# Kernel tuning notes

Measured on AMD Instinct MI355X. Metric: run time of the kernel, lower is better.

The kernel has to match this reference:

```python
import jax, jax.numpy as jnp
import numpy as np

EPS = 1e-6
ROPE_THETA = 1000000.0
SPAN_LENGTHS = [700, 300, 600, 448]
L, D, H, HK, DH, FF = 2, 2048, 16, 8, 128, 8192


def _rmsnorm(x, w):
    var = jnp.mean(jnp.square(x), axis=-1, keepdims=True)
    return x * jax.lax.rsqrt(var + EPS) * w


def _rotate_half(x):
    x1, x2 = jnp.split(x, 2, axis=-1)
    return jnp.concatenate([-x2, x1], axis=-1)


def setup_inputs() -> dict:
    key = jax.random.key(0)
    ks = jax.random.split(key, 8)
    s = 0.02  # init scale
    seg = np.repeat(np.arange(len(SPAN_LENGTHS), dtype=np.int32), SPAN_LENGTHS)
    pos = np.concatenate([np.arange(n, dtype=np.int32) for n in SPAN_LENGTHS])
    T = seg.shape[0]
    return {
        "hidden_states": jax.random.normal(ks[0], (T, D), jnp.float32),
        "ln1_w": jnp.ones((L, D), jnp.float32),
        "ln2_w": jnp.ones((L, D), jnp.float32),
        "wq": jax.random.normal(ks[1], (L, D, H * DH), jnp.float32) * s,
        "wk": jax.random.normal(ks[2], (L, D, HK * DH), jnp.float32) * s,
        "wv": jax.random.normal(ks[3], (L, D, HK * DH), jnp.float32) * s,
        "wo": jax.random.normal(ks[4], (L, H * DH, D), jnp.float32) * s,
        "qn_w": jnp.ones((L, DH), jnp.float32),
        "kn_w": jnp.ones((L, DH), jnp.float32),
        "wg": jax.random.normal(ks[5], (L, D, FF), jnp.float32) * s,
        "wu": jax.random.normal(ks[6], (L, D, FF), jnp.float32) * s,
        "wd": jax.random.normal(ks[7], (L, FF, D), jnp.float32) * s,
        "final_norm_w": jnp.ones((D,), jnp.float32),
        "segment_ids": jnp.asarray(seg),
        "position_ids": jnp.asarray(pos),
    }


def reference(hidden_states, ln1_w, ln2_w, wq, wk, wv, wo, qn_w, kn_w, wg, wu, wd, final_norm_w, segment_ids, position_ids):
    T = hidden_states.shape[0]
    # rotary tables from per-request positions (positions reset per span)
    inv_freq = 1.0 / (ROPE_THETA ** (jnp.arange(0, DH, 2, dtype=jnp.float32) / DH))
    freqs = position_ids.astype(jnp.float32)[:, None] * inv_freq  # [T, DH/2]
    emb = jnp.concatenate([freqs, freqs], axis=-1)                # [T, DH]
    cos = jnp.cos(emb)[:, None, :]
    sin = jnp.sin(emb)[:, None, :]
    # ragged causal mask: attend only within the same request span, causally
    tok = jnp.arange(T)
    mask = (segment_ids[:, None] == segment_ids[None, :]) & (tok[:, None] >= tok[None, :])
    neg = jnp.finfo(hidden_states.dtype).min
    scale = 1.0 / np.sqrt(DH)

    x = hidden_states
    for l in range(L):
        h = _rmsnorm(x, ln1_w[l])
        q = (h @ wq[l]).reshape(T, H, DH)
        k = (h @ wk[l]).reshape(T, HK, DH)
        v = (h @ wv[l]).reshape(T, HK, DH)
        q = _rmsnorm(q, qn_w[l])  # Qwen3 per-head q/k RMSNorm
        k = _rmsnorm(k, kn_w[l])
        q = q * cos + _rotate_half(q) * sin
        k = k * cos + _rotate_half(k) * sin
        rep = H // HK  # GQA
        k = jnp.repeat(k, rep, axis=1)
        v = jnp.repeat(v, rep, axis=1)
        scores = jnp.einsum('thd,shd->hts', q, k) * scale  # [H, T, T]
        scores = jnp.where(mask[None], scores, neg)
        attn = jax.nn.softmax(scores, axis=-1)
        o = jnp.einsum('hts,shd->thd', attn, v).reshape(T, H * DH)
        x = x + o @ wo[l]
        h = _rmsnorm(x, ln2_w[l])
        x = x + (jax.nn.silu(h @ wg[l]) * (h @ wu[l])) @ wd[l]
    return _rmsnorm(x, final_norm_w)
```

## Files before the change

### kernel.cpp

```cpp
#include <hip/hip_runtime.h>
#include <stdint.h>

#define T_SEQ 2048
#define DMODEL 2048
#define NH 16
#define NKV 8
#define DHEAD 128
#define DFF 8192

typedef float f32x4 __attribute__((ext_vector_type(4)));
typedef float f32x2 __attribute__((ext_vector_type(2)));
typedef __bf16 bf16x8 __attribute__((ext_vector_type(8)));
typedef unsigned short ushort_t;

typedef __attribute__((address_space(1))) void gvoid;
typedef __attribute__((address_space(3))) void lvoid;

__device__ inline unsigned short f2bf(float f) {
  unsigned int u = __float_as_uint(f);
  u += 0x7fffu + ((u >> 16) & 1u);
  return (unsigned short)(u >> 16);
}
__device__ inline float bf2f(unsigned short h) {
  return __uint_as_float(((unsigned int)h) << 16);
}

__device__ inline void gload_lds16(const void* g, void* l) {
  __builtin_amdgcn_global_load_lds((gvoid*)g, (lvoid*)l, 16, 0, 0);
}

template <typename TIN>
__global__ __launch_bounds__(256) void k_transpose_bf16(const TIN* __restrict__ in,
                                                        ushort_t* __restrict__ out,
                                                        int R, int C) {
  __shared__ float tile[64 * 72];
  int tid = threadIdx.x;
  int r0 = blockIdx.y * 64, c0 = blockIdx.x * 64;
  int rl = tid >> 4;
  int cc = tid & 15;
#pragma unroll
  for (int i = 0; i < 4; ++i) {
    int row = rl + i * 16;
    const TIN* src = in + (size_t)(r0 + row) * C + c0 + cc * 4;
    float v0, v1, v2, v3;
    if constexpr (sizeof(TIN) == 4) {
      f32x4 v = *(const f32x4*)src;
      v0 = v.x; v1 = v.y; v2 = v.z; v3 = v.w;
    } else {
      ushort4 v = *(const ushort4*)src;
      v0 = bf2f(v.x); v1 = bf2f(v.y); v2 = bf2f(v.z); v3 = bf2f(v.w);
    }
    int chunk = cc ^ (row & 15);
    f32x4 t = {v0, v1, v2, v3};
    *(f32x4*)&tile[row * 72 + chunk * 4] = t;
  }
  __syncthreads();
#pragma unroll
  for (int i = 0; i < 4; ++i) {
    int nrow = rl + i * 16;
    int k4 = cc * 4;
    ushort4 o;
    {
      int k = k4 + 0;
      o.x = f2bf(tile[k * 72 + (((nrow >> 2) ^ (k & 15)) << 2) + (nrow & 3)]);
      k = k4 + 1;
      o.y = f2bf(tile[k * 72 + (((nrow >> 2) ^ (k & 15)) << 2) + (nrow & 3)]);
      k = k4 + 2;
      o.z = f2bf(tile[k * 72 + (((nrow >> 2) ^ (k & 15)) << 2) + (nrow & 3)]);
      k = k4 + 3;
      o.w = f2bf(tile[k * 72 + (((nrow >> 2) ^ (k & 15)) << 2) + (nrow & 3)]);
    }
    *(ushort4*)(out + (size_t)(c0 + nrow) * R + r0 + k4) = o;
  }
}

template <int BF16OUT>
__global__ __launch_bounds__(256) void k_rmsnorm(const float* __restrict__ X,
                                                 const float* __restrict__ W,
                                                 void* __restrict__ OUT) {
  int row = blockIdx.x, tid = threadIdx.x;
  const float* xr = X + (size_t)row * DMODEL;
  f32x4 x0 = *(const f32x4*)(xr + tid * 4);
  f32x4 x1 = *(const f32x4*)(xr + 1024 + tid * 4);
  float ss = x0.x * x0.x + x0.y * x0.y + x0.z * x0.z + x0.w * x0.w +
             x1.x * x1.x + x1.y * x1.y + x1.z * x1.z + x1.w * x1.w;
#pragma unroll
  for (int o = 1; o < 64; o <<= 1) ss += __shfl_xor(ss, o, 64);
  __shared__ float red[4];
  int w = tid >> 6;
  if ((tid & 63) == 0) red[w] = ss;
  __syncthreads();
  float tot = red[0] + red[1] + red[2] + red[3];
  float sc = rsqrtf(tot / (float)DMODEL + 1e-6f);
  f32x4 w0 = *(const f32x4*)(W + tid * 4);
  f32x4 w1 = *(const f32x4*)(W + 1024 + tid * 4);
  if constexpr (BF16OUT) {
    ushort_t* o = (ushort_t*)OUT + (size_t)row * DMODEL;
    ushort4 a, b;
    a.x = f2bf(x0.x * sc * w0.x); a.y = f2bf(x0.y * sc * w0.y);
    a.z = f2bf(x0.z * sc * w0.z); a.w = f2bf(x0.w * sc * w0.w);
    b.x = f2bf(x1.x * sc * w1.x); b.y = f2bf(x1.y * sc * w1.y);
    b.z = f2bf(x1.z * sc * w1.z); b.w = f2bf(x1.w * sc * w1.w);
    *(ushort4*)(o + tid * 4) = a;
    *(ushort4*)(o + 1024 + tid * 4) = b;
  } else {
    float* o = (float*)OUT + (size_t)row * DMODEL;
    f32x4 a = {x0.x * sc * w0.x, x0.y * sc * w0.y, x0.z * sc * w0.z, x0.w * sc * w0.w};
    f32x4 b = {x1.x * sc * w1.x, x1.y * sc * w1.y, x1.z * sc * w1.z, x1.w * sc * w1.w};
    *(f32x4*)(o + tid * 4) = a;
    *(f32x4*)(o + 1024 + tid * 4) = b;
  }
}

__global__ __launch_bounds__(256) void k_red4res(const float* __restrict__ P,
                                                 const float* __restrict__ RES,
                                                 float* __restrict__ OUT, int n) {
  int i = (blockIdx.x * 256 + threadIdx.x) * 4;
  if (i >= n) return;
  f32x4 v = *(const f32x4*)(RES + i);
#pragma unroll
  for (int z = 0; z < 4; ++z) {
    f32x4 t = *(const f32x4*)(P + (size_t)z * n + i);
    v.x += t.x; v.y += t.y; v.z += t.z; v.w += t.w;
  }
  *(f32x4*)(OUT + i) = v;
}

#define EPI_STORE 0
#define EPI_SILU 2
#define EPI_STOREB 3

#define LOAD_B256(bs, rbase)                                                   \
  {                                                                            \
    _Pragma("unroll") for (int ks = 0; ks < 2; ++ks)                           \
        _Pragma("unroll") for (int ni = 0; ni < 2; ++ni)                       \
            bfr[ks][ni] = *(const bf16x8*)((bs) +                              \
                (((rbase) + ni * 16 + lr) << 6) +                              \
                ((((ks << 2) + lg) ^ (lr & 7)) << 3));                         \
  }

#define MFMA_Q256(q)                                                           \
  {                                                                            \
    _Pragma("unroll") for (int ks = 0; ks < 2; ++ks)                           \
        _Pragma("unroll") for (int mi = 0; mi < 4; ++mi)                       \
            _Pragma("unroll") for (int ni = 0; ni < 2; ++ni)                   \
                acc[mi][(q) * 2 + ni] =                                        \
                    __builtin_amdgcn_mfma_f32_16x16x32_bf16(                   \
                        af[ks][mi], bfr[ks][ni], acc[mi][(q) * 2 + ni], 0, 0, 0); \
  }

template <int LAST>
__device__ __forceinline__ void g256_iter(
    const ushort_t* __restrict__ as, const ushort_t* __restrict__ bsA,
    const ushort_t* __restrict__ bsB, ushort_t* __restrict__ nA,
    ushort_t* __restrict__ nB, const ushort_t* __restrict__ an,
    const ushort_t* __restrict__ bn, size_t rs, int slds, int lr, int lg,
    f32x4 (&acc)[4][8]) {
  bf16x8 af[2][4], bfr[2][2];
#pragma unroll
  for (int ks = 0; ks < 2; ++ks)
#pragma unroll
    for (int mi = 0; mi < 4; ++mi)
      af[ks][mi] = *(const bf16x8*)(as + ((mi * 16 + lr) << 6) +
                                    ((((ks << 2) + lg) ^ (lr & 7)) << 3));
  LOAD_B256(bsA, 0);
  if constexpr (!LAST) {
    gload_lds16(an, nA + slds);
    gload_lds16(an + rs, nA + 4096 + slds);
  }
  __builtin_amdgcn_s_barrier();
  asm volatile("s_waitcnt lgkmcnt(0)" ::: "memory");
  __builtin_amdgcn_sched_barrier(0);
  __builtin_amdgcn_s_setprio(1);
  MFMA_Q256(0);
  __builtin_amdgcn_s_setprio(0);
  __builtin_amdgcn_s_barrier();
  LOAD_B256(bsA, 32);
  if constexpr (!LAST) {
    gload_lds16(an + 2 * rs, nA + 8192 + slds);
    gload_lds16(an + 3 * rs, nA + 12288 + slds);
    asm volatile("s_waitcnt vmcnt(4)" ::: "memory");
  } else {
    asm volatile("s_waitcnt vmcnt(0)" ::: "memory");
  }
  __builtin_amdgcn_s_barrier();
  asm volatile("s_waitcnt lgkmcnt(0)" ::: "memory");
  __builtin_amdgcn_sched_barrier(0);
  __builtin_amdgcn_s_setprio(1);
  MFMA_Q256(1);
  __builtin_amdgcn_s_setprio(0);
  __builtin_amdgcn_s_barrier();
  LOAD_B256(bsB, 0);
  if constexpr (!LAST) {
    gload_lds16(bn, nB + slds);
    gload_lds16(bn + 2 * rs, nB + 8192 + slds);
  }
  __builtin_amdgcn_s_barrier();
  asm volatile("s_waitcnt lgkmcnt(0)" ::: "memory");
  __builtin_amdgcn_sched_barrier(0);
  __builtin_amdgcn_s_setprio(1);
  MFMA_Q256(2);
  __builtin_amdgcn_s_setprio(0);
  __builtin_amdgcn_s_barrier();
  LOAD_B256(bsB, 32);
  if constexpr (!LAST) {
    gload_lds16(bn + rs, nB + 4096 + slds);
    gload_lds16(bn + 3 * rs, nB + 12288 + slds);
    asm volatile("s_waitcnt vmcnt(2)" ::: "memory");
  }
  __builtin_amdgcn_s_barrier();
  asm volatile("s_waitcnt lgkmcnt(0)" ::: "memory");
  __builtin_amdgcn_sched_barrier(0);
  __builtin_amdgcn_s_setprio(1);
  MFMA_Q256(3);
  __builtin_amdgcn_s_setprio(0);
  __builtin_amdgcn_s_barrier();
}

template <int EPI>
__global__ __launch_bounds__(512, 2) void k_gemm256(
    const ushort_t* __restrict__ A, const ushort_t* __restrict__ BT,
    const ushort_t* __restrict__ GINB, float* __restrict__ CF,
    ushort_t* __restrict__ CB, int N, int Kstride, int Kc, size_t zoff) {
  __shared__ ushort_t lds[65536];
  const int tid = threadIdx.x;
  const int l = tid & 63, wid = tid >> 6;
  const int wm = wid >> 1, wn = wid & 1;
  const int lr = l & 15, lg = l >> 4;
  const int m0 = blockIdx.y * 256, n0 = blockIdx.x * 256;
  const int z = blockIdx.z;
  const int NT = Kc >> 6;

  A += (size_t)z * Kc;
  BT += (size_t)z * Kc;
  CF += (size_t)z * zoff;

  const int srow = tid >> 3;
  const int scs = (tid & 7) ^ (srow & 7);
  const size_t sgoff = (size_t)srow * Kstride + scs * 8;
  const int slds = wid * 512;

  const ushort_t* ga = A + (size_t)m0 * Kstride + sgoff;
  const ushort_t* gb = BT + (size_t)n0 * Kstride + sgoff;
  const size_t rs = (size_t)64 * Kstride;

  f32x4 acc[4][8] = {};

  ushort_t* Ab0 = lds;
  ushort_t* Bb0 = lds + 16384;
  ushort_t* Ab1 = lds + 32768;
  ushort_t* Bb1 = lds + 49152;

  gload_lds16(ga, Ab0 + slds);
  gload_lds16(ga + rs, Ab0 + 4096 + slds);
  gload_lds16(ga + 2 * rs, Ab0 + 8192 + slds);
  gload_lds16(ga + 3 * rs, Ab0 + 12288 + slds);
  gload_lds16(gb, Bb0 + slds);
  gload_lds16(gb + 2 * rs, Bb0 + 8192 + slds);
  gload_lds16(gb + rs, Bb0 + 4096 + slds);
  gload_lds16(gb + 3 * rs, Bb0 + 12288 + slds);
  asm volatile("s_waitcnt vmcnt(2)" ::: "memory");
  __builtin_amdgcn_s_barrier();

  for (int kt = 0; kt < NT - 1; ++kt) {
    const int d = kt & 1;
    const ushort_t* as = (d ? Ab1 : Ab0) + wm * 4096;
    const ushort_t* bsA = (d ? Bb1 : Bb0) + (wn * 2) * 4096;
    ushort_t* nA = d ? Ab0 : Ab1;
    ushort_t* nB = d ? Bb0 : Bb1;
    g256_iter<0>(as, bsA, bsA + 4096, nA, nB, ga + (size_t)(kt + 1) * 64,
                 gb + (size_t)(kt + 1) * 64, rs, slds, lr, lg, acc);
  }
  {
    const int d = (NT - 1) & 1;
    const ushort_t* as = (d ? Ab1 : Ab0) + wm * 4096;
    const ushort_t* bsA = (d ? Bb1 : Bb0) + (wn * 2) * 4096;
    g256_iter<1>(as, bsA, bsA + 4096, nullptr, nullptr, nullptr, nullptr, rs,
                 slds, lr, lg, acc);
  }

#pragma unroll
  for (int mi = 0; mi < 4; ++mi)
#pragma unroll
    for (int ci = 0; ci < 8; ++ci)
#pragma unroll
      for (int rr = 0; rr < 4; ++rr) {
        int m = m0 + wm * 64 + mi * 16 + lg * 4 + rr;
        int n = n0 + wn * 128 + ci * 16 + lr;
        size_t off = (size_t)m * N + n;
        float v = acc[mi][ci][rr];
        if constexpr (EPI == EPI_STORE) {
          CF[off] = v;
        } else if constexpr (EPI == EPI_STOREB) {
          CB[off] = f2bf(v);
        } else {
          float gv = bf2f(GINB[off]);
          float s = gv / (1.f + __expf(-gv));
          CB[off] = f2bf(s * v);
        }
      }
}

__global__ __launch_bounds__(256) void k_qkv_post(const float* __restrict__ Q0,
                                                  const float* __restrict__ Q1,
                                                  const float* __restrict__ QNW,
                                                  const float* __restrict__ KNW,
                                                  const int* __restrict__ POS,
                                                  ushort_t* __restrict__ Qb,
                                                  ushort_t* __restrict__ Kb,
                                                  ushort_t* __restrict__ Vb) {
  int t = blockIdx.x;
  int tid = threadIdx.x;
  int w = tid >> 6, l = tid & 63;
  float pos = (float)POS[t];
  const float* base0 = Q0 + (size_t)t * 4096;
  const float* base1 = Q1 + (size_t)t * 4096;
  int i0 = 2 * (l & 31);
  const float K2 = 19.931568569324174f / 64.f;
  float ang0 = pos * exp2f(-(float)i0 * K2);
  float ang1 = pos * exp2f(-(float)(i0 + 1) * K2);
  float cs0 = cosf(ang0), sn0 = sinf(ang0);
  float cs1 = cosf(ang1), sn1 = sinf(ang1);
#pragma unroll
  for (int si = 0; si < 8; ++si) {
    int slot = w + si * 4;
    f32x2 xa = *(const f32x2*)(base0 + slot * 128 + l * 2);
    f32x2 xb = *(const f32x2*)(base1 + slot * 128 + l * 2);
    float v0 = xa.x + xb.x, v1 = xa.y + xb.y;
    float ss = v0 * v0 + v1 * v1;
#pragma unroll
    for (int o = 1; o < 64; o <<= 1) ss += __shfl_xor(ss, o, 64);
    if (slot < 24) {
      float sc = rsqrtf(ss / 128.f + 1e-6f);
      const float* wn = (slot < 16) ? QNW : KNW;
      f32x2 wv = *(const f32x2*)(wn + l * 2);
      v0 = v0 * sc * wv.x;
      v1 = v1 * sc * wv.y;
      float p0 = __shfl_xor(v0, 32, 64);
      float p1 = __shfl_xor(v1, 32, 64);
      float r0 = (l < 32) ? -p0 : p0;
      float r1 = (l < 32) ? -p1 : p1;
      v0 = v0 * cs0 + r0 * sn0;
      v1 = v1 * cs1 + r1 * sn1;
    }
    ushort2 uv;
    uv.x = f2bf(v0);
    uv.y = f2bf(v1);
    ushort_t* dst;
    if (slot < 16)
      dst = Qb + (size_t)t * 2048 + slot * 128 + l * 2;
    else if (slot < 24)
      dst = Kb + (size_t)t * 1024 + (slot - 16) * 128 + l * 2;
    else
      dst = Vb + (size_t)t * 1024 + (slot - 24) * 128 + l * 2;
    *(ushort2*)dst = uv;
  }
}

__global__ __launch_bounds__(64) void k_flash(const ushort_t* __restrict__ Qb,
                                              const ushort_t* __restrict__ Kb,
                                              const ushort_t* __restrict__ VT,
                                              const int* __restrict__ SEG,
                                              ushort_t* __restrict__ Ob) {
  __shared__ ushort_t Pl[16 * 40];
  int l = threadIdx.x;
  int qt = blockIdx.x, h = blockIdx.y;
  int q0 = qt * 16;
  int lr = l & 15, lg = l >> 4;
  int kvh = h >> 1;
  bf16x8 qf[4];
  {
    const bf16x8* qv = (const bf16x8*)(Qb + (size_t)(q0 + lr) * 2048 + h * 128);
#pragma unroll
    for (int kk = 0; kk < 4; ++kk) qf[kk] = qv[kk * 4 + lg];
  }
  int segq[4];
#pragma unroll
  for (int r = 0; r < 4; ++r) segq[r] = SEG[q0 + lg * 4 + r];
  int target = SEG[q0];
  int lo = 0, hi = q0;
  while (lo < hi) {
    int mid = (lo + hi) >> 1;
    if (SEG[mid] < target) lo = mid + 1; else hi = mid;
  }
  int s_start = lo & ~31;
  float m_run[4], l_run[4];
  f32x4 acc[8] = {};
#pragma unroll
  for (int r = 0; r < 4; ++r) { m_run[r] = -1e30f; l_run[r] = 0.f; }
  const float scale = 0.08838834764831845f;
  for (int s0 = s_start; s0 < q0 + 16; s0 += 32) {
    int sa = s0 + lr, sb = s0 + 16 + lr;
    int sac = min(sa, T_SEQ - 1), sbc = min(sb, T_SEQ - 1);
    f32x4 SA = {}, SB = {};
    const bf16x8* ka = (const bf16x8*)(Kb + (size_t)sac * 1024 + kvh * 128);
    const bf16x8* kb = (const bf16x8*)(Kb + (size_t)sbc * 1024 + kvh * 128);
#pragma unroll
    for (int kk = 0; kk < 4; ++kk) {
      SA = __builtin_amdgcn_mfma_f32_16x16x32_bf16(qf[kk], ka[kk * 4 + lg], SA, 0, 0, 0);
      SB = __builtin_amdgcn_mfma_f32_16x16x32_bf16(qf[kk], kb[kk * 4 + lg], SB, 0, 0, 0);
    }
    int sga = SEG[sac], sgb = SEG[sbc];
    float al[4], pA[4], pB[4];
#pragma unroll
    for (int r = 0; r < 4; ++r) {
      int qrow = q0 + lg * 4 + r;
      float xa = (sa <= qrow && sga == segq[r]) ? SA[r] * scale : -1e30f;
      float xb = (sb <= qrow && sgb == segq[r]) ? SB[r] * scale : -1e30f;
      float mx = fmaxf(xa, xb);
#pragma unroll
      for (int o = 1; o < 16; o <<= 1) mx = fmaxf(mx, __shfl_xor(mx, o, 64));
      float nm = fmaxf(m_run[r], mx);
      float ea = __expf(xa - nm), eb = __expf(xb - nm);
      float rs = ea + eb;
#pragma unroll
      for (int o = 1; o < 16; o <<= 1) rs += __shfl_xor(rs, o, 64);
      al[r] = __expf(m_run[r] - nm);
      l_run[r] = l_run[r] * al[r] + rs;
      m_run[r] = nm;
      pA[r] = ea;
      pB[r] = eb;
    }
#pragma unroll
    for (int c = 0; c < 8; ++c)
#pragma unroll
      for (int r = 0; r < 4; ++r) acc[c][r] *= al[r];
    __syncthreads();
#pragma unroll
    for (int r = 0; r < 4; ++r) {
      Pl[(lg * 4 + r) * 40 + lr] = f2bf(pA[r]);
      Pl[(lg * 4 + r) * 40 + 16 + lr] = f2bf(pB[r]);
    }
    __syncthreads();
    bf16x8 pa = *(const bf16x8*)&Pl[lr * 40 + lg * 8];
    int sbase = min(s0 + lg * 8, T_SEQ - 8);
#pragma unroll
    for (int c = 0; c < 8; ++c) {
      bf16x8 vb = *(const bf16x8*)(VT + (size_t)(kvh * 128 + c * 16 + lr) * T_SEQ + sbase);
      acc[c] = __builtin_amdgcn_mfma_f32_16x16x32_bf16(pa, vb, acc[c], 0, 0, 0);
    }
  }
#pragma unroll
  for (int c = 0; c < 8; ++c)
#pragma unroll
    for (int r = 0; r < 4; ++r) {
      float ov = acc[c][r] / l_run[r];
      Ob[(size_t)(q0 + lg * 4 + r) * 2048 + h * 128 + c * 16 + lr] = f2bf(ov);
    }
}

extern "C" void kernel_launch(void* const* d_in, const int* in_sizes, int n_in,
                              void* d_out, int out_size, void* d_ws, size_t ws_size,
                              hipStream_t stream) {
  const float* hidden = (const float*)d_in[0];
  const float* ln1 = (const float*)d_in[1];
  const float* ln2 = (const float*)d_in[2];
  const float* wq = (const float*)d_in[3];
  const float* wk = (const float*)d_in[4];
  const float* wv = (const float*)d_in[5];
  const float* wo = (const float*)d_in[6];
  const float* qnw = (const float*)d_in[7];
  const float* knw = (const float*)d_in[8];
  const float* wg = (const float*)d_in[9];
  const float* wu = (const float*)d_in[10];
  const float* wd = (const float*)d_in[11];
  const float* fnw = (const float*)d_in[12];
  const int* seg = (const int*)d_in[13];
  const int* pos = (const int*)d_in[14];
  float* out = (float*)d_out;

  char* ws = (char*)d_ws;
  size_t off = 0;
  auto alloc = [&](size_t bytes) {
    char* p = ws + off;
    off += (bytes + 255) & ~(size_t)255;
    return p;
  };
  ushort_t* wT = (ushort_t*)alloc((size_t)DFF * DMODEL * 2);
  ushort_t* hbuf = (ushort_t*)alloc((size_t)T_SEQ * DMODEL * 2);
  ushort_t* qb = (ushort_t*)alloc((size_t)T_SEQ * 2048 * 2);
  ushort_t* kb = (ushort_t*)alloc((size_t)T_SEQ * 1024 * 2);
  ushort_t* vb = (ushort_t*)alloc((size_t)T_SEQ * 1024 * 2);
  ushort_t* vT = (ushort_t*)alloc((size_t)T_SEQ * 1024 * 2);
  ushort_t* ob = (ushort_t*)alloc((size_t)T_SEQ * 2048 * 2);
  float* gbufF = (float*)alloc((size_t)T_SEQ * DFF * 4);
  ushort_t* gbufB = (ushort_t*)gbufF;
  ushort_t* mbuf = (ushort_t*)alloc((size_t)T_SEQ * DFF * 2);
  (void)ws_size; (void)in_sizes; (void)n_in; (void)out_size;

  dim3 b256(256), b64(64), b512(512);
  for (int lyr = 0; lyr < 2; ++lyr) {
    const float* xsrc = (lyr == 0) ? hidden : out;
    k_rmsnorm<1><<<T_SEQ, b256, 0, stream>>>(xsrc, ln1 + (size_t)lyr * DMODEL, hbuf);

    const float* wql = wq + (size_t)lyr * DMODEL * 2048;
    const float* wkl = wk + (size_t)lyr * DMODEL * 1024;
    const float* wvl = wv + (size_t)lyr * DMODEL * 1024;
    k_transpose_bf16<float><<<dim3(32, 32), b256, 0, stream>>>(wql, wT, 2048, 2048);
    k_transpose_bf16<float><<<dim3(16, 32), b256, 0, stream>>>(wkl, wT + (size_t)2048 * 2048, 2048, 1024);
    k_transpose_bf16<float><<<dim3(16, 32), b256, 0, stream>>>(wvl, wT + (size_t)3072 * 2048, 2048, 1024);
    k_gemm256<EPI_STORE><<<dim3(16, 8, 2), b512, 0, stream>>>(
        hbuf, wT, nullptr, gbufF, nullptr, 4096, 2048, 1024, (size_t)2048 * 4096);
    k_qkv_post<<<T_SEQ, b256, 0, stream>>>(gbufF, gbufF + (size_t)2048 * 4096,
                                           qnw + (size_t)lyr * 128, knw + (size_t)lyr * 128,
                                           pos, qb, kb, vb);
    k_transpose_bf16<ushort_t><<<dim3(16, 32), b256, 0, stream>>>(vb, vT, 2048, 1024);
    k_flash<<<dim3(T_SEQ / 16, NH), b64, 0, stream>>>(qb, kb, vT, seg, ob);

    const float* wol = wo + (size_t)lyr * 2048 * DMODEL;
    k_transpose_bf16<float><<<dim3(32, 32), b256, 0, stream>>>(wol, wT, 2048, 2048);
    k_gemm256<EPI_STORE><<<dim3(8, 8, 4), b512, 0, stream>>>(
        ob, wT, nullptr, gbufF, nullptr, 2048, 2048, 512, (size_t)2048 * 2048);
    k_red4res<<<4096, b256, 0, stream>>>(gbufF, xsrc, out, 2048 * 2048);

    k_rmsnorm<1><<<T_SEQ, b256, 0, stream>>>(out, ln2 + (size_t)lyr * DMODEL, hbuf);

    const float* wgl = wg + (size_t)lyr * DMODEL * DFF;
    const float* wul = wu + (size_t)lyr * DMODEL * DFF;
    const float* wdl = wd + (size_t)lyr * DFF * DMODEL;
    k_transpose_bf16<float><<<dim3(128, 32), b256, 0, stream>>>(wgl, wT, 2048, 8192);
    k_gemm256<EPI_STOREB><<<dim3(32, 8, 1), b512, 0, stream>>>(
        hbuf, wT, nullptr, nullptr, gbufB, 8192, 2048, 2048, 0);
    k_transpose_bf16<float><<<dim3(128, 32), b256, 0, stream>>>(wul, wT, 2048, 8192);
    k_gemm256<EPI_SILU><<<dim3(32, 8, 1), b512, 0, stream>>>(
        hbuf, wT, gbufB, nullptr, mbuf, 8192, 2048, 2048, 0);
    k_transpose_bf16<float><<<dim3(32, 128), b256, 0, stream>>>(wdl, wT, 8192, 2048);
    k_gemm256<EPI_STORE><<<dim3(8, 8, 4), b512, 0, stream>>>(
        mbuf, wT, nullptr, gbufF, nullptr, 2048, 8192, 2048, (size_t)2048 * 2048);
    k_red4res<<<4096, b256, 0, stream>>>(gbufF, out, out, 2048 * 2048);
  }
  k_rmsnorm<0><<<T_SEQ, b256, 0, stream>>>(out, fnw, out);
}
```

Measured before the change: 986.0 us.

## Store GEMM partials in bf16, fuse residual reduce with RMSNorm, share KV across heads

Split-K GEMM partial outputs, including the QKV partials, are now written as bf16 instead of fp32, which halves the traffic for the partial store and reload. The residual reduction now also computes the following RMSNorm in one kernel, removing the separate norm launches. The flash attention kernel now processes both query heads of a GQA group per block, so K and V loads are shared, and V is prefetched before the softmax. This drops the LDS barriers but adds register pressure, and bf16 partials reduce accuracy.

```diff
diff --git a/kernel.cpp b/kernel.cpp
--- a/kernel.cpp
+++ b/kernel.cpp
@@ -112,21 +112,40 @@
   }
 }
 
-__global__ __launch_bounds__(256) void k_red4res(const float* __restrict__ P,
-                                                 const float* __restrict__ RES,
-                                                 float* __restrict__ OUT, int n) {
-  int i = (blockIdx.x * 256 + threadIdx.x) * 4;
-  if (i >= n) return;
-  f32x4 v = *(const f32x4*)(RES + i);
-#pragma unroll
-  for (int z = 0; z < 4; ++z) {
-    f32x4 t = *(const f32x4*)(P + (size_t)z * n + i);
-    v.x += t.x; v.y += t.y; v.z += t.z; v.w += t.w;
-  }
-  *(f32x4*)(OUT + i) = v;
-}
-
-#define EPI_STORE 0
+template <int NZ, int WRITEH>
+__global__ __launch_bounds__(512) void k_redln(const ushort_t* __restrict__ P,
+                                               const float* __restrict__ RES,
+                                               const float* __restrict__ W,
+                                               float* __restrict__ OUT,
+                                               ushort_t* __restrict__ HB) {
+  int row = blockIdx.x, tid = threadIdx.x;
+  size_t base = (size_t)row * DMODEL + tid * 4;
+  f32x4 v = *(const f32x4*)(RES + base);
+#pragma unroll
+  for (int z = 0; z < NZ; ++z) {
+    ushort4 t = *(const ushort4*)(P + (size_t)z * T_SEQ * DMODEL + base);
+    v.x += bf2f(t.x); v.y += bf2f(t.y); v.z += bf2f(t.z); v.w += bf2f(t.w);
+  }
+  *(f32x4*)(OUT + base) = v;
+  if constexpr (WRITEH) {
+    float ss = v.x * v.x + v.y * v.y + v.z * v.z + v.w * v.w;
+#pragma unroll
+    for (int o = 1; o < 64; o <<= 1) ss += __shfl_xor(ss, o, 64);
+    __shared__ float red[8];
+    if ((tid & 63) == 0) red[tid >> 6] = ss;
+    __syncthreads();
+    float tot = 0.f;
+#pragma unroll
+    for (int i = 0; i < 8; ++i) tot += red[i];
+    float sc = rsqrtf(tot / (float)DMODEL + 1e-6f);
+    f32x4 wv = *(const f32x4*)(W + tid * 4);
+    ushort4 h;
+    h.x = f2bf(v.x * sc * wv.x); h.y = f2bf(v.y * sc * wv.y);
+    h.z = f2bf(v.z * sc * wv.z); h.w = f2bf(v.w * sc * wv.w);
+    *(ushort4*)(HB + base) = h;
+  }
+}
+
 #define EPI_SILU 2
 #define EPI_STOREB 3
 
@@ -220,8 +239,8 @@
 template <int EPI>
 __global__ __launch_bounds__(512, 2) void k_gemm256(
     const ushort_t* __restrict__ A, const ushort_t* __restrict__ BT,
-    const ushort_t* __restrict__ GINB, float* __restrict__ CF,
-    ushort_t* __restrict__ CB, int N, int Kstride, int Kc, size_t zoff) {
+    const ushort_t* __restrict__ GINB, ushort_t* __restrict__ CB,
+    int N, int Kstride, int Kc, size_t zoff) {
   __shared__ ushort_t lds[65536];
   const int tid = threadIdx.x;
   const int l = tid & 63, wid = tid >> 6;
@@ -233,7 +252,7 @@
 
   A += (size_t)z * Kc;
   BT += (size_t)z * Kc;
-  CF += (size_t)z * zoff;
+  CB += (size_t)z * zoff;
 
   const int srow = tid >> 3;
   const int scs = (tid & 7) ^ (srow & 7);
@@ -289,9 +308,7 @@
         int n = n0 + wn * 128 + ci * 16 + lr;
         size_t off = (size_t)m * N + n;
         float v = acc[mi][ci][rr];
-        if constexpr (EPI == EPI_STORE) {
-          CF[off] = v;
-        } else if constexpr (EPI == EPI_STOREB) {
+        if constexpr (EPI == EPI_STOREB) {
           CB[off] = f2bf(v);
         } else {
           float gv = bf2f(GINB[off]);
@@ -301,8 +318,8 @@
       }
 }
 
-__global__ __launch_bounds__(256) void k_qkv_post(const float* __restrict__ Q0,
-                                                  const float* __restrict__ Q1,
+__global__ __launch_bounds__(256) void k_qkv_post(const ushort_t* __restrict__ Q0,
+                                                  const ushort_t* __restrict__ Q1,
                                                   const float* __restrict__ QNW,
                                                   const float* __restrict__ KNW,
                                                   const int* __restrict__ POS,
@@ -313,8 +330,8 @@
   int tid = threadIdx.x;
   int w = tid >> 6, l = tid & 63;
   float pos = (float)POS[t];
-  const float* base0 = Q0 + (size_t)t * 4096;
-  const float* base1 = Q1 + (size_t)t * 4096;
+  const ushort_t* base0 = Q0 + (size_t)t * 4096;
+  const ushort_t* base1 = Q1 + (size_t)t * 4096;
   int i0 = 2 * (l & 31);
   const float K2 = 19.931568569324174f / 64.f;
   float ang0 = pos * exp2f(-(float)i0 * K2);
@@ -324,9 +341,9 @@
 #pragma unroll
   for (int si = 0; si < 8; ++si) {
     int slot = w + si * 4;
-    f32x2 xa = *(const f32x2*)(base0 + slot * 128 + l * 2);
-    f32x2 xb = *(const f32x2*)(base1 + slot * 128 + l * 2);
-    float v0 = xa.x + xb.x, v1 = xa.y + xb.y;
+    ushort2 xa = *(const ushort2*)(base0 + slot * 128 + l * 2);
+    ushort2 xb = *(const ushort2*)(base1 + slot * 128 + l * 2);
+    float v0 = bf2f(xa.x) + bf2f(xb.x), v1 = bf2f(xa.y) + bf2f(xb.y);
     float ss = v0 * v0 + v1 * v1;
 #pragma unroll
     for (int o = 1; o < 64; o <<= 1) ss += __shfl_xor(ss, o, 64);
@@ -362,17 +379,20 @@
                                               const ushort_t* __restrict__ VT,
                                               const int* __restrict__ SEG,
                                               ushort_t* __restrict__ Ob) {
-  __shared__ ushort_t Pl[16 * 40];
+  __shared__ ushort_t Pl[2][16 * 40];
   int l = threadIdx.x;
-  int qt = blockIdx.x, h = blockIdx.y;
+  int qt = blockIdx.x, kvh = blockIdx.y;
   int q0 = qt * 16;
   int lr = l & 15, lg = l >> 4;
-  int kvh = h >> 1;
-  bf16x8 qf[4];
+  int h0 = kvh * 2;
+  bf16x8 qf0[4], qf1[4];
   {
-    const bf16x8* qv = (const bf16x8*)(Qb + (size_t)(q0 + lr) * 2048 + h * 128);
-#pragma unroll
-    for (int kk = 0; kk < 4; ++kk) qf[kk] = qv[kk * 4 + lg];
+    const bf16x8* qv = (const bf16x8*)(Qb + (size_t)(q0 + lr) * 2048 + h0 * 128);
+#pragma unroll
+    for (int kk = 0; kk < 4; ++kk) {
+      qf0[kk] = qv[kk * 4 + lg];
+      qf1[kk] = qv[16 + kk * 4 + lg];
+    }
   }
   int segq[4];
 #pragma unroll
@@ -384,69 +404,84 @@
     if (SEG[mid] < target) lo = mid + 1; else hi = mid;
   }
   int s_start = lo & ~31;
-  float m_run[4], l_run[4];
-  f32x4 acc[8] = {};
-#pragma unroll
-  for (int r = 0; r < 4; ++r) { m_run[r] = -1e30f; l_run[r] = 0.f; }
+  float mr[2][4], lrun[2][4];
+  f32x4 acc[2][8] = {};
+#pragma unroll
+  for (int h = 0; h < 2; ++h)
+#pragma unroll
+    for (int r = 0; r < 4; ++r) { mr[h][r] = -1e30f; lrun[h][r] = 0.f; }
   const float scale = 0.08838834764831845f;
   for (int s0 = s_start; s0 < q0 + 16; s0 += 32) {
     int sa = s0 + lr, sb = s0 + 16 + lr;
     int sac = min(sa, T_SEQ - 1), sbc = min(sb, T_SEQ - 1);
-    f32x4 SA = {}, SB = {};
+    bf16x8 vfr[8];
+    int sbase = min(s0 + lg * 8, T_SEQ - 8);
+#pragma unroll
+    for (int c = 0; c < 8; ++c)
+      vfr[c] = *(const bf16x8*)(VT + (size_t)(kvh * 128 + c * 16 + lr) * T_SEQ + sbase);
+    f32x4 SA0 = {}, SB0 = {}, SA1 = {}, SB1 = {};
     const bf16x8* ka = (const bf16x8*)(Kb + (size_t)sac * 1024 + kvh * 128);
-    const bf16x8* kb = (const bf16x8*)(Kb + (size_t)sbc * 1024 + kvh * 128);
+    const bf16x8* kb_ = (const bf16x8*)(Kb + (size_t)sbc * 1024 + kvh * 128);
 #pragma unroll
     for (int kk = 0; kk < 4; ++kk) {
-      SA = __builtin_amdgcn_mfma_f32_16x16x32_bf16(qf[kk], ka[kk * 4 + lg], SA, 0, 0, 0);
-      SB = __builtin_amdgcn_mfma_f32_16x16x32_bf16(qf[kk], kb[kk * 4 + lg], SB, 0, 0, 0);
+      bf16x8 kaf = ka[kk * 4 + lg];
+      bf16x8 kbf = kb_[kk * 4 + lg];
+      SA0 = __builtin_amdgcn_mfma_f32_16x16x32_bf16(qf0[kk], kaf, SA0, 0, 0, 0);
+      SB0 = __builtin_amdgcn_mfma_f32_16x16x32_bf16(qf0[kk], kbf, SB0, 0, 0, 0);
+      SA1 = __builtin_amdgcn_mfma_f32_16x16x32_bf16(qf1[kk], kaf, SA1, 0, 0, 0);
+      SB1 = __builtin_amdgcn_mfma_f32_16x16x32_bf16(qf1[kk], kbf, SB1, 0, 0, 0);
     }
     int sga = SEG[sac], sgb = SEG[sbc];
-    float al[4], pA[4], pB[4];
+    bool mAv[4], mBv[4];
 #pragma unroll
     for (int r = 0; r < 4; ++r) {
       int qrow = q0 + lg * 4 + r;
-      float xa = (sa <= qrow && sga == segq[r]) ? SA[r] * scale : -1e30f;
-      float xb = (sb <= qrow && sgb == segq[r]) ? SB[r] * scale : -1e30f;
-      float mx = fmaxf(xa, xb);
-#pragma unroll
-      for (int o = 1; o < 16; o <<= 1) mx = fmaxf(mx, __shfl_xor(mx, o, 64));
-      float nm = fmaxf(m_run[r], mx);
-      float ea = __expf(xa - nm), eb = __expf(xb - nm);
-      float rs = ea + eb;
-#pragma unroll
-      for (int o = 1; o < 16; o <<= 1) rs += __shfl_xor(rs, o, 64);
-      al[r] = __expf(m_run[r] - nm);
-      l_run[r] = l_run[r] * al[r] + rs;
-      m_run[r] = nm;
-      pA[r] = ea;
-      pB[r] = eb;
-    }
+      mAv[r] = (sa <= qrow) && (sga == segq[r]);
+      mBv[r] = (sb <= qrow) && (sgb == segq[r]);
+    }
+#pragma unroll
+    for (int h = 0; h < 2; ++h) {
+#pragma unroll
+      for (int r = 0; r < 4; ++r) {
+        float sva = (h ? SA1[r] : SA0[r]);
+        float svb = (h ? SB1[r] : SB0[r]);
+        float xa = mAv[r] ? sva * scale : -1e30f;
+        float xb = mBv[r] ? svb * scale : -1e30f;
+        float mx = fmaxf(xa, xb);
+#pragma unroll
+        for (int o = 1; o < 16; o <<= 1) mx = fmaxf(mx, __shfl_xor(mx, o, 64));
+        float nm = fmaxf(mr[h][r], mx);
+        float ea = __expf(xa - nm), eb = __expf(xb - nm);
+        float rsum = ea + eb;
+#pragma unroll
+        for (int o = 1; o < 16; o <<= 1) rsum += __shfl_xor(rsum, o, 64);
+        float al = __expf(mr[h][r] - nm);
+        lrun[h][r] = lrun[h][r] * al + rsum;
+        mr[h][r] = nm;
+#pragma unroll
+        for (int c = 0; c < 8; ++c) acc[h][c][r] *= al;
+        Pl[h][(lg * 4 + r) * 40 + lr] = f2bf(ea);
+        Pl[h][(lg * 4 + r) * 40 + 16 + lr] = f2bf(eb);
+      }
+    }
+    asm volatile("s_waitcnt lgkmcnt(0)" ::: "memory");
+    bf16x8 pa0 = *(const bf16x8*)&Pl[0][lr * 40 + lg * 8];
+    bf16x8 pa1 = *(const bf16x8*)&Pl[1][lr * 40 + lg * 8];
+#pragma unroll
+    for (int c = 0; c < 8; ++c) {
+      acc[0][c] = __builtin_amdgcn_mfma_f32_16x16x32_bf16(pa0, vfr[c], acc[0][c], 0, 0, 0);
+      acc[1][c] = __builtin_amdgcn_mfma_f32_16x16x32_bf16(pa1, vfr[c], acc[1][c], 0, 0, 0);
+    }
+  }
+#pragma unroll
+  for (int h = 0; h < 2; ++h)
 #pragma unroll
     for (int c = 0; c < 8; ++c)
 #pragma unroll
-      for (int r = 0; r < 4; ++r) acc[c][r] *= al[r];
-    __syncthreads();
-#pragma unroll
-    for (int r = 0; r < 4; ++r) {
-      Pl[(lg * 4 + r) * 40 + lr] = f2bf(pA[r]);
-      Pl[(lg * 4 + r) * 40 + 16 + lr] = f2bf(pB[r]);
-    }
-    __syncthreads();
-    bf16x8 pa = *(const bf16x8*)&Pl[lr * 40 + lg * 8];
-    int sbase = min(s0 + lg * 8, T_SEQ - 8);
-#pragma unroll
-    for (int c = 0; c < 8; ++c) {
-      bf16x8 vb = *(const bf16x8*)(VT + (size_t)(kvh * 128 + c * 16 + lr) * T_SEQ + sbase);
-      acc[c] = __builtin_amdgcn_mfma_f32_16x16x32_bf16(pa, vb, acc[c], 0, 0, 0);
-    }
-  }
-#pragma unroll
-  for (int c = 0; c < 8; ++c)
-#pragma unroll
-    for (int r = 0; r < 4; ++r) {
-      float ov = acc[c][r] / l_run[r];
-      Ob[(size_t)(q0 + lg * 4 + r) * 2048 + h * 128 + c * 16 + lr] = f2bf(ov);
-    }
+      for (int r = 0; r < 4; ++r) {
+        float ov = acc[h][c][r] / lrun[h][r];
+        Ob[(size_t)(q0 + lg * 4 + r) * 2048 + (h0 + h) * 128 + c * 16 + lr] = f2bf(ov);
+      }
 }
 
 extern "C" void kernel_launch(void* const* d_in, const int* in_sizes, int n_in,
@@ -483,15 +518,17 @@
   ushort_t* vb = (ushort_t*)alloc((size_t)T_SEQ * 1024 * 2);
   ushort_t* vT = (ushort_t*)alloc((size_t)T_SEQ * 1024 * 2);
   ushort_t* ob = (ushort_t*)alloc((size_t)T_SEQ * 2048 * 2);
-  float* gbufF = (float*)alloc((size_t)T_SEQ * DFF * 4);
-  ushort_t* gbufB = (ushort_t*)gbufF;
+  ushort_t* qkvp = (ushort_t*)alloc((size_t)2 * T_SEQ * 4096 * 2);
+  ushort_t* pbuf = (ushort_t*)alloc((size_t)4 * T_SEQ * DMODEL * 2);
+  ushort_t* gbufB = (ushort_t*)alloc((size_t)T_SEQ * DFF * 2);
   ushort_t* mbuf = (ushort_t*)alloc((size_t)T_SEQ * DFF * 2);
   (void)ws_size; (void)in_sizes; (void)n_in; (void)out_size;
 
   dim3 b256(256), b64(64), b512(512);
+  k_rmsnorm<1><<<T_SEQ, b256, 0, stream>>>(hidden, ln1, hbuf);
+
   for (int lyr = 0; lyr < 2; ++lyr) {
     const float* xsrc = (lyr == 0) ? hidden : out;
-    k_rmsnorm<1><<<T_SEQ, b256, 0, stream>>>(xsrc, ln1 + (size_t)lyr * DMODEL, hbuf);
 
     const float* wql = wq + (size_t)lyr * DMODEL * 2048;
     const float* wkl = wk + (size_t)lyr * DMODEL * 1024;
@@ -499,35 +536,38 @@
     k_transpose_bf16<float><<<dim3(32, 32), b256, 0, stream>>>(wql, wT, 2048, 2048);
     k_transpose_bf16<float><<<dim3(16, 32), b256, 0, stream>>>(wkl, wT + (size_t)2048 * 2048, 2048, 1024);
     k_transpose_bf16<float><<<dim3(16, 32), b256, 0, stream>>>(wvl, wT + (size_t)3072 * 2048, 2048, 1024);
-    k_gemm256<EPI_STORE><<<dim3(16, 8, 2), b512, 0, stream>>>(
-        hbuf, wT, nullptr, gbufF, nullptr, 4096, 2048, 1024, (size_t)2048 * 4096);
-    k_qkv_post<<<T_SEQ, b256, 0, stream>>>(gbufF, gbufF + (size_t)2048 * 4096,
+    k_gemm256<EPI_STOREB><<<dim3(16, 8, 2), b512, 0, stream>>>(
+        hbuf, wT, nullptr, qkvp, 4096, 2048, 1024, (size_t)2048 * 4096);
+    k_qkv_post<<<T_SEQ, b256, 0, stream>>>(qkvp, qkvp + (size_t)2048 * 4096,
                                            qnw + (size_t)lyr * 128, knw + (size_t)lyr * 128,
                                            pos, qb, kb, vb);
     k_transpose_bf16<ushort_t><<<dim3(16, 32), b256, 0, stream>>>(vb, vT, 2048, 1024);
-    k_flash<<<dim3(T_SEQ / 16, NH), b64, 0, stream>>>(qb, kb, vT, seg, ob);
+    k_flash<<<dim3(T_SEQ / 16, NKV), b64, 0, stream>>>(qb, kb, vT, seg, ob);
 
     const float* wol = wo + (size_t)lyr * 2048 * DMODEL;
     k_transpose_bf16<float><<<dim3(32, 32), b256, 0, stream>>>(wol, wT, 2048, 2048);
-    k_gemm256<EPI_STORE><<<dim3(8, 8, 4), b512, 0, stream>>>(
-        ob, wT, nullptr, gbufF, nullptr, 2048, 2048, 512, (size_t)2048 * 2048);
-    k_red4res<<<4096, b256, 0, stream>>>(gbufF, xsrc, out, 2048 * 2048);
-
-    k_rmsnorm<1><<<T_SEQ, b256, 0, stream>>>(out, ln2 + (size_t)lyr * DMODEL, hbuf);
+    k_gemm256<EPI_STOREB><<<dim3(8, 8, 4), b512, 0, stream>>>(
+        ob, wT, nullptr, pbuf, 2048, 2048, 512, (size_t)2048 * 2048);
+    k_redln<4, 1><<<T_SEQ, b512, 0, stream>>>(pbuf, xsrc,
+                                              ln2 + (size_t)lyr * DMODEL, out, hbuf);
 
     const float* wgl = wg + (size_t)lyr * DMODEL * DFF;
     const float* wul = wu + (size_t)lyr * DMODEL * DFF;
     const float* wdl = wd + (size_t)lyr * DFF * DMODEL;
     k_transpose_bf16<float><<<dim3(128, 32), b256, 0, stream>>>(wgl, wT, 2048, 8192);
     k_gemm256<EPI_STOREB><<<dim3(32, 8, 1), b512, 0, stream>>>(
-        hbuf, wT, nullptr, nullptr, gbufB, 8192, 2048, 2048, 0);
+        hbuf, wT, nullptr, gbufB, 8192, 2048, 2048, 0);
     k_transpose_bf16<float><<<dim3(128, 32), b256, 0, stream>>>(wul, wT, 2048, 8192);
     k_gemm256<EPI_SILU><<<dim3(32, 8, 1), b512, 0, stream>>>(
-        hbuf, wT, gbufB, nullptr, mbuf, 8192, 2048, 2048, 0);
+        hbuf, wT, gbufB, mbuf, 8192, 2048, 2048, 0);
     k_transpose_bf16<float><<<dim3(32, 128), b256, 0, stream>>>(wdl, wT, 8192, 2048);
-    k_gemm256<EPI_STORE><<<dim3(8, 8, 4), b512, 0, stream>>>(
-        mbuf, wT, nullptr, gbufF, nullptr, 2048, 8192, 2048, (size_t)2048 * 2048);
-    k_red4res<<<4096, b256, 0, stream>>>(gbufF, out, out, 2048 * 2048);
+    k_gemm256<EPI_STOREB><<<dim3(8, 8, 4), b512, 0, stream>>>(
+        mbuf, wT, nullptr, pbuf, 2048, 8192, 2048, (size_t)2048 * 2048);
+    if (lyr == 0) {
+      k_redln<4, 1><<<T_SEQ, b512, 0, stream>>>(pbuf, out, ln1 + DMODEL, out, hbuf);
+    } else {
+      k_redln<4, 0><<<T_SEQ, b512, 0, stream>>>(pbuf, out, nullptr, out, nullptr);
+    }
   }
   k_rmsnorm<0><<<T_SEQ, b256, 0, stream>>>(out, fnw, out);
 }
```

Result: faster. 893.8 us (-9.4%).
